# Kernel tuning notes

Hardware: AMD Instinct MI355X
Metric: run time of the kernel (lower is better)

Reference implementation:

```python
import math
import jax, jax.numpy as jnp
import numpy as np

HIDDEN = 768
N_HEADS = 12
HEAD_DIM = HIDDEN // N_HEADS


def _alibi_slopes(num_heads: int) -> np.ndarray:
    def pow2_slopes(n):
        start = 2.0 ** (-2.0 ** (-(math.log2(n) - 3)))
        return start ** np.arange(1, n + 1, dtype=np.float32)
    if math.log2(num_heads).is_integer():
        return pow2_slopes(num_heads).astype(np.float32)
    closest = 2 ** math.floor(math.log2(num_heads))
    base = pow2_slopes(closest)
    extra = pow2_slopes(2 * closest)[0::2][: num_heads - closest]
    return np.concatenate([base, extra], axis=0).astype(np.float32)

ALIBI_SLOPES = jnp.asarray(_alibi_slopes(N_HEADS))


def setup_inputs() -> dict:
    key = jax.random.key(0)
    ks = jax.random.split(key, 7)
    B, S = 4, 2048
    scale = 1.0 / math.sqrt(HIDDEN)
    inp = {
        "hidden_states": jax.random.normal(ks[0], (B, S, HIDDEN), dtype=jnp.float32),
        "Wq": jax.random.normal(ks[1], (HIDDEN, HIDDEN), dtype=jnp.float32) * scale,
        "bq": jnp.zeros((HIDDEN,), dtype=jnp.float32),
        "Wk": jax.random.normal(ks[2], (HIDDEN, HIDDEN), dtype=jnp.float32) * scale,
        "bk": jnp.zeros((HIDDEN,), dtype=jnp.float32),
        "Wv": jax.random.normal(ks[3], (HIDDEN, HIDDEN), dtype=jnp.float32) * scale,
        "bv": jnp.zeros((HIDDEN,), dtype=jnp.float32),
        "attention_mask": jnp.ones((B, S), dtype=jnp.int32),
    }
    return inp


def reference(hidden_states, Wq, bq, Wk, bk, Wv, bv, attention_mask):
    B, S, _ = hidden_states.shape
    H, D = N_HEADS, HEAD_DIM
    scaling = D ** (-0.5)

    # nn.Linear: x @ W.T + b, then split heads -> [B, S, H, D]
    q = (hidden_states @ Wq.T + bq).reshape(B, S, H, D)
    k = (hidden_states @ Wk.T + bk).reshape(B, S, H, D)
    v = (hidden_states @ Vv_fix(Wv, bv, hidden_states)) if False else (hidden_states @ Wv.T + bv).reshape(B, S, H, D)

    # scaled scores [B, H, Sq, Sk]
    scores = jnp.einsum("bqhd,bkhd->bhqk", q, k) * scaling

    # ALiBi bias: -slope[h] * |kv_idx - q_idx|
    pos = jnp.arange(S)
    dist = jnp.abs(pos[None, :] - pos[:, None]).astype(scores.dtype)  # [Sq, Sk]
    alibi = -ALIBI_SLOPES.astype(scores.dtype)[:, None, None] * dist  # [H, Sq, Sk]

    # padding mask over kv positions (additive min like score_mod)
    mask_penalty = jnp.finfo(scores.dtype).min
    mask_bias = jnp.where(attention_mask.astype(bool), 0.0, mask_penalty)  # [B, Sk]

    scores = scores + alibi[None] + mask_bias[:, None, None, :]
    probs = jax.nn.softmax(scores, axis=-1)

    out = jnp.einsum("bhqk,bkhd->bqhd", probs, v)  # [B, Sq, H, D]
    return out.reshape(B, S, H * D)  # dropout is no-op in eval


def Vv_fix(*a):  # unused helper kept trivially (never called)
    raise NotImplementedError
```

## Files before the change

kernel.cpp:

```cpp
#include <hip/hip_runtime.h>
#include <hip/hip_bf16.h>

#define HIDDEN 768
#define NH 12
#define HD 64
#define BB 4
#define SS 2048
#define M_TOT (BB * SS)
#define NQKV (3 * HIDDEN)
#define LOG2E 1.44269504f

typedef __attribute__((ext_vector_type(8))) short bf16x8;
typedef __attribute__((ext_vector_type(4))) float f32x4;
typedef __attribute__((ext_vector_type(4))) unsigned int u32x4;

__device__ inline unsigned short f2bf(float x) {
    __hip_bfloat16 h = __float2bfloat16(x);
    return *reinterpret_cast<unsigned short*>(&h);
}

__device__ inline void gl_lds16(const unsigned short* g, unsigned short* s) {
    __builtin_amdgcn_global_load_lds(
        (const __attribute__((address_space(1))) unsigned int*)g,
        (__attribute__((address_space(3))) unsigned int*)s, 16, 0, 0);
}

__device__ inline void bar_vm4() {
    __builtin_amdgcn_sched_barrier(0);
    asm volatile("s_waitcnt vmcnt(4)" ::: "memory");
    __builtin_amdgcn_s_barrier();
    __builtin_amdgcn_sched_barrier(0);
}
__device__ inline void bar_vm0() {
    __builtin_amdgcn_sched_barrier(0);
    asm volatile("s_waitcnt vmcnt(0)" ::: "memory");
    __builtin_amdgcn_s_barrier();
    __builtin_amdgcn_sched_barrier(0);
}

__global__ __launch_bounds__(256) void cast_kernel(
    const float* __restrict__ hs, const float* __restrict__ wq,
    const float* __restrict__ wk, const float* __restrict__ wv,
    const int* __restrict__ mask, unsigned short* __restrict__ a_bf,
    unsigned short* __restrict__ w_bf, float* __restrict__ mb,
    int* __restrict__ anym) {
    const int HS_N = M_TOT * HIDDEN / 4;
    const int W_N = HIDDEN * HIDDEN / 4;
    int idx = blockIdx.x * blockDim.x + threadIdx.x;
    if (idx < BB * SS) mb[idx] = mask[idx] ? 0.f : -1e30f;
    if (idx < BB * 32) {
        int b = idx >> 5, t = idx & 31;
        const int* mp = mask + b * SS + t * 64;
        int any = 0;
#pragma unroll 8
        for (int j = 0; j < 64; j++) any |= (mp[j] == 0);
        anym[idx] = any;
    }
    if (idx >= HS_N + 3 * W_N) return;
    if (idx < HS_N) {
        float4 v = ((const float4*)hs)[idx];
        ushort4 o;
        o.x = f2bf(v.x); o.y = f2bf(v.y); o.z = f2bf(v.z); o.w = f2bf(v.w);
        ((ushort4*)a_bf)[idx] = o;
    } else {
        int widx = idx - HS_N;
        const float* src;
        int off;
        if (widx < W_N)        { src = wq; off = widx; }
        else if (widx < 2*W_N) { src = wk; off = widx - W_N; }
        else                   { src = wv; off = widx - 2 * W_N; }
        float4 v = ((const float4*)src)[off];
        ushort4 o;
        o.x = f2bf(v.x); o.y = f2bf(v.y); o.z = f2bf(v.z); o.w = f2bf(v.w);
        ((ushort4*)w_bf)[widx] = o;
    }
}

__global__ __launch_bounds__(256, 3) void qkv_gemm(
    const unsigned short* __restrict__ A, const unsigned short* __restrict__ W,
    const float* __restrict__ bq, const float* __restrict__ bk,
    const float* __restrict__ bv, unsigned short* __restrict__ qbuf,
    unsigned short* __restrict__ kf, unsigned short* __restrict__ vf) {
    __shared__ unsigned short As[3][128][32];
    __shared__ unsigned short Bs[3][128][32];
    const int tid = threadIdx.x;
    const int flat = blockIdx.y * gridDim.x + blockIdx.x;
    const int xcd = flat & 7;
    const int qq = flat >> 3;
    const int mgrp = qq / 18;
    const int nidx = qq % 18;
    const int m0 = (mgrp * 8 + xcd) * 128;
    const int n0 = nidx * 128;
    const int w = tid >> 6, l = tid & 63;
    const int wm = w >> 1, wn = w & 1;
    const int lrow = l & 15;
    const int g4 = l >> 4;
    const int fcol = (g4 ^ (lrow >> 2)) * 8;

    const int srow = l >> 2;
    const int sslot = (l & 3) ^ ((l >> 4) & 3);
    const unsigned short* pA =
        A + (size_t)(m0 + w * 32 + srow) * HIDDEN + sslot * 8;
    const unsigned short* pB =
        W + (size_t)(n0 + w * 32 + srow) * HIDDEN + sslot * 8;

    f32x4 acc[4][4] = {};

#define STAGE(bb)                                          \
    do {                                                   \
        gl_lds16(pA,               &As[bb][w * 32][0]);    \
        gl_lds16(pA + 16 * HIDDEN, &As[bb][w * 32 + 16][0]); \
        gl_lds16(pB,               &Bs[bb][w * 32][0]);    \
        gl_lds16(pB + 16 * HIDDEN, &Bs[bb][w * 32 + 16][0]); \
        pA += 32; pB += 32;                                \
    } while (0)

    STAGE(0);
    STAGE(1);
    bar_vm4();
    int cur = 0;
    const int NKT = HIDDEN / 32;

    for (int kt = 0; kt < NKT; kt++) {
        if (kt + 2 < NKT) {
            int db = (cur >= 1) ? cur - 1 : 2;
            STAGE(db);
        }
        bf16x8 af[4], bfr[4];
#pragma unroll
        for (int mi = 0; mi < 4; mi++)
            af[mi] = *(const bf16x8*)&As[cur][wm * 64 + mi * 16 + lrow][fcol];
#pragma unroll
        for (int ni = 0; ni < 4; ni++)
            bfr[ni] = *(const bf16x8*)&Bs[cur][wn * 64 + ni * 16 + lrow][fcol];
        __builtin_amdgcn_s_setprio(1);
#pragma unroll
        for (int mi = 0; mi < 4; mi++)
#pragma unroll
            for (int ni = 0; ni < 4; ni++)
                acc[mi][ni] = __builtin_amdgcn_mfma_f32_16x16x32_bf16(
                    af[mi], bfr[ni], acc[mi][ni], 0, 0, 0);
        __builtin_amdgcn_s_setprio(0);
        if (kt < NKT - 1) {
            if (kt < NKT - 2) bar_vm4();
            else bar_vm0();
        }
        cur = (cur == 2) ? 0 : cur + 1;
    }
#undef STAGE

    if (n0 < 768) {
#pragma unroll
        for (int mi = 0; mi < 4; mi++) {
            const size_t rbase =
                (size_t)(m0 + wm * 64 + mi * 16 + g4 * 4) * 768;
#pragma unroll
            for (int ni = 0; ni < 4; ni++) {
                int col = n0 + wn * 64 + ni * 16 + lrow;
                float bias = bq[col];
#pragma unroll
                for (int i = 0; i < 4; i++)
                    qbuf[rbase + (size_t)i * 768 + col] =
                        f2bf((acc[mi][ni][i] + bias) * 0.125f);
            }
        }
    } else if (n0 < 1536) {
        const int bb2 = m0 >> 11;
        const int sbase = (m0 & 2047) + wm * 64 + g4 * 4;
        const int lsb = g4 * 4;
#pragma unroll
        for (int mi = 0; mi < 4; mi++) {
            const int kv16 = (sbase + mi * 16) >> 4;
#pragma unroll
            for (int ni = 0; ni < 4; ni++) {
                int dd = n0 - 768 + wn * 64 + ni * 16 + lrow;
                float bias = bk[dd];
                int hh = dd >> 6, d = dd & 63;
                int gk2 = d >> 3, d8 = d & 7;
                size_t base = ((size_t)(bb2 * NH + hh) * 128 + kv16) * 1024 +
                              (gk2 * 16 + lsb) * 8 + d8;
#pragma unroll
                for (int i = 0; i < 4; i++)
                    kf[base + i * 8] = f2bf(acc[mi][ni][i] + bias);
            }
        }
    } else {
        const int bb2 = m0 >> 11;
#pragma unroll
        for (int mi = 0; mi < 4; mi++) {
            const int s0r = (m0 & 2047) + wm * 64 + mi * 16 + g4 * 4;
            const int kv32 = s0r >> 5, gv = (s0r >> 3) & 3, s8 = s0r & 7;
#pragma unroll
            for (int ni = 0; ni < 4; ni++) {
                int dd = n0 - 1536 + wn * 64 + ni * 16 + lrow;
                float bias = bv[dd];
                int hh = dd >> 6, d = dd & 63;
                int dm = d >> 4, lr = d & 15;
                ushort4 o;
                o.x = f2bf(acc[mi][ni][0] + bias);
                o.y = f2bf(acc[mi][ni][1] + bias);
                o.z = f2bf(acc[mi][ni][2] + bias);
                o.w = f2bf(acc[mi][ni][3] + bias);
                *(ushort4*)(vf + (((size_t)(bb2 * NH + hh) * 4 + dm) * 64 + kv32) * 512 +
                            (gv * 16 + lr) * 8 + s8) = o;
            }
        }
    }
}

__global__ __launch_bounds__(256) void attn_kernel(
    const unsigned short* __restrict__ Qb, const unsigned short* __restrict__ KF,
    const unsigned short* __restrict__ VF, const float* __restrict__ MB,
    const int* __restrict__ ANYM, float* __restrict__ out) {
    __shared__ unsigned short Kl[2][4096];
    __shared__ unsigned short Vl[2][4096];

    const int head_order[12] = {7, 6, 5, 4, 3, 11, 2, 10, 1, 9, 0, 8};
    const int Rtab[12]       = {31, 17, 9, 5, 3, 2, 2, 1, 1, 1, 1, 1};

    const int tid = threadIdx.x;
    const int w = tid >> 6, l = tid & 63;
    const int flat = blockIdx.y * gridDim.x + blockIdx.x;
    const int xcd = flat & 7;
    const int rem = flat >> 3;
    const int slot = rem >> 5;
    const int qt = rem & 31;
    const int byy = slot * 8 + xcd;
    const int hidx = byy >> 2;
    const int b = byy & 3;
    const int h = head_order[hidx];
    const int R = Rtab[hidx];
    const int bh = b * NH + h;
    const int lrow = l & 15;
    const int g = l >> 4;
    const int q = qt * 64 + w * 16 + lrow;
    const int l8 = l * 8;

    const float slope = (h < 8) ? exp2f(-(float)(h + 1))
                                : exp2f(-((float)(h - 8) + 0.5f));
    const float nslope2 = -slope * LOG2E;
    const float stp = 64.f * nslope2;

    const unsigned short* qp = Qb + (size_t)(b * SS + q) * 768 + h * HD + g * 8;
    const bf16x8 qf0 = *(const bf16x8*)(qp);
    const bf16x8 qf1 = *(const bf16x8*)(qp + 32);

    const unsigned short* kfb = KF + (size_t)bh * 128 * 1024;
    const unsigned short* vfb = VF + (size_t)bh * 4 * 64 * 512;
    const float* mbp = MB + b * SS + g * 4;
    const int* anyp = ANYM + b * 32;

    bf16x8 ones;
#pragma unroll
    for (int j = 0; j < 8; j++) ones[j] = (short)0x3F80;

    f32x4 accT[4] = {};
    f32x4 lacc = {};
    float m_run = 14.0f;
    float ta[16];
    bool need_full = true;

    const int kt_lo = max(0, qt - R);
    const int kt_hi = min(31, qt + R);

    {
        const unsigned short* gk0 = kfb + ((size_t)kt_lo * 4 + w) * 1024 + l8;
        const unsigned short* gv0 = vfb + ((size_t)w * 64 + kt_lo * 2) * 512 + l8;
        gl_lds16(gk0,       &Kl[0][w * 1024]);
        gl_lds16(gk0 + 512, &Kl[0][w * 1024 + 512]);
        gl_lds16(gv0,       &Vl[0][w * 1024]);
        gl_lds16(gv0 + 512, &Vl[0][w * 1024 + 512]);
    }
    __syncthreads();

    const unsigned short* gk = kfb + ((size_t)(kt_lo + 1) * 4 + w) * 1024 + l8;
    const unsigned short* gv = vfb + ((size_t)w * 64 + (size_t)(kt_lo + 1) * 2) * 512 + l8;
    int cur = 0;

    for (int kt = kt_lo; kt <= kt_hi; kt++) {
        if (kt < kt_hi) {
            gl_lds16(gk,       &Kl[cur ^ 1][w * 1024]);
            gl_lds16(gk + 512, &Kl[cur ^ 1][w * 1024 + 512]);
            gl_lds16(gv,       &Vl[cur ^ 1][w * 1024]);
            gl_lds16(gv + 512, &Vl[cur ^ 1][w * 1024 + 512]);
            gk += 4096;
            gv += 1024;
        }

        f32x4 s4[4];
        __builtin_amdgcn_s_setprio(1);
#pragma unroll
        for (int nf = 0; nf < 4; nf++) {
            bf16x8 k0 = *(const bf16x8*)&Kl[cur][nf * 1024 + l8];
            bf16x8 k1 = *(const bf16x8*)&Kl[cur][nf * 1024 + 512 + l8];
            f32x4 z = {};
            z = __builtin_amdgcn_mfma_f32_16x16x32_bf16(k0, qf0, z, 0, 0, 0);
            z = __builtin_amdgcn_mfma_f32_16x16x32_bf16(k1, qf1, z, 0, 0, 0);
            s4[nf] = z;
        }
        __builtin_amdgcn_s_setprio(0);

        if (need_full || kt == qt || kt == qt + 1) {
            const float fdf = (float)(kt * 64 + g * 4 - q);
#pragma unroll
            for (int nf = 0; nf < 4; nf++)
#pragma unroll
                for (int i = 0; i < 4; i++)
                    ta[nf * 4 + i] = fabsf(fdf + (float)(nf * 16 + i)) * nslope2;
        } else {
            const float d = (kt > qt) ? stp : -stp;
#pragma unroll
            for (int e = 0; e < 16; e++) ta[e] += d;
        }
        need_full = false;

        float sv[16];
#pragma unroll
        for (int nf = 0; nf < 4; nf++)
#pragma unroll
            for (int i = 0; i < 4; i++)
                sv[nf * 4 + i] = fmaf(s4[nf][i], LOG2E, ta[nf * 4 + i]);
        if (anyp[kt]) {
#pragma unroll
            for (int nf = 0; nf < 4; nf++) {
                float4 mbv = *(const float4*)(mbp + kt * 64 + nf * 16);
                sv[nf * 4 + 0] += mbv.x;
                sv[nf * 4 + 1] += mbv.y;
                sv[nf * 4 + 2] += mbv.z;
                sv[nf * 4 + 3] += mbv.w;
            }
        }

        float t0 = fmaxf(fmaxf(sv[0], sv[1]), sv[2]);
        float t1 = fmaxf(fmaxf(sv[3], sv[4]), sv[5]);
        float t2 = fmaxf(fmaxf(sv[6], sv[7]), sv[8]);
        float t3 = fmaxf(fmaxf(sv[9], sv[10]), sv[11]);
        float t4 = fmaxf(fmaxf(sv[12], sv[13]), sv[14]);
        float mt = fmaxf(fmaxf(fmaxf(t0, t1), fmaxf(t2, t3)), fmaxf(t4, sv[15]));

        if (!__all(mt <= m_run + 8.0f)) {
            mt = fmaxf(mt, __shfl_xor(mt, 16));
            mt = fmaxf(mt, __shfl_xor(mt, 32));
            mt = fmaxf(mt, __shfl_xor(mt, 1));
            mt = fmaxf(mt, __shfl_xor(mt, 2));
            mt = fmaxf(mt, __shfl_xor(mt, 4));
            mt = fmaxf(mt, __shfl_xor(mt, 8));
            float mnew = fmaxf(m_run, mt);
            float corr = __builtin_amdgcn_exp2f(m_run - mnew);
            m_run = mnew;
#pragma unroll
            for (int i = 0; i < 4; i++) lacc[i] *= corr;
#pragma unroll
            for (int m = 0; m < 4; m++)
#pragma unroll
                for (int i = 0; i < 4; i++) accT[m][i] *= corr;
        }

        float p[16];
#pragma unroll
        for (int e = 0; e < 16; e++)
            p[e] = __builtin_amdgcn_exp2f(sv[e] - m_run);

        unsigned pk[4][2];
#pragma unroll
        for (int nf = 0; nf < 4; nf++) {
            asm("v_cvt_pk_bf16_f32 %0, %1, %2"
                : "=v"(pk[nf][0]) : "v"(p[nf * 4 + 0]), "v"(p[nf * 4 + 1]));
            asm("v_cvt_pk_bf16_f32 %0, %1, %2"
                : "=v"(pk[nf][1]) : "v"(p[nf * 4 + 2]), "v"(p[nf * 4 + 3]));
        }

        const int dstA = ((((g & 1) << 1) | (g >> 1)) << 4) | lrow;
        const int idxA = dstA << 2;
        const int idxB = idxA ^ 128;
        const bool odd = (g & 1);
        unsigned rA0 = __builtin_amdgcn_ds_permute(idxA, (int)(odd ? pk[1][0] : pk[0][0]));
        unsigned rA1 = __builtin_amdgcn_ds_permute(idxA, (int)(odd ? pk[1][1] : pk[0][1]));
        unsigned rB0 = __builtin_amdgcn_ds_permute(idxB, (int)(odd ? pk[0][0] : pk[1][0]));
        unsigned rB1 = __builtin_amdgcn_ds_permute(idxB, (int)(odd ? pk[0][1] : pk[1][1]));
        unsigned rA2 = __builtin_amdgcn_ds_permute(idxA, (int)(odd ? pk[3][0] : pk[2][0]));
        unsigned rA3 = __builtin_amdgcn_ds_permute(idxA, (int)(odd ? pk[3][1] : pk[2][1]));
        unsigned rB2 = __builtin_amdgcn_ds_permute(idxB, (int)(odd ? pk[2][0] : pk[3][0]));
        unsigned rB3 = __builtin_amdgcn_ds_permute(idxB, (int)(odd ? pk[2][1] : pk[3][1]));
        const bool hi = (g >> 1);
        u32x4 uf0, uf1;
        uf0.x = hi ? rB0 : rA0; uf0.y = hi ? rB1 : rA1;
        uf0.z = hi ? rA0 : rB0; uf0.w = hi ? rA1 : rB1;
        uf1.x = hi ? rB2 : rA2; uf1.y = hi ? rB3 : rA3;
        uf1.z = hi ? rA2 : rB2; uf1.w = hi ? rA3 : rB3;
        bf16x8 pf0 = __builtin_bit_cast(bf16x8, uf0);
        bf16x8 pf1 = __builtin_bit_cast(bf16x8, uf1);

        __builtin_amdgcn_s_setprio(1);
#pragma unroll
        for (int m = 0; m < 4; m++) {
            bf16x8 v0 = *(const bf16x8*)&Vl[cur][m * 1024 + l8];
            bf16x8 v1 = *(const bf16x8*)&Vl[cur][m * 1024 + 512 + l8];
            accT[m] = __builtin_amdgcn_mfma_f32_16x16x32_bf16(v0, pf0, accT[m], 0, 0, 0);
            accT[m] = __builtin_amdgcn_mfma_f32_16x16x32_bf16(v1, pf1, accT[m], 0, 0, 0);
        }
        lacc = __builtin_amdgcn_mfma_f32_16x16x32_bf16(ones, pf0, lacc, 0, 0, 0);
        lacc = __builtin_amdgcn_mfma_f32_16x16x32_bf16(ones, pf1, lacc, 0, 0, 0);
        __builtin_amdgcn_s_setprio(0);

        __syncthreads();
        cur ^= 1;
    }

    const float inv = 1.0f / lacc[0];
    float* op = out + (size_t)(b * SS + q) * HIDDEN + h * HD + g * 4;
#pragma unroll
    for (int m = 0; m < 4; m++) {
        float4 o;
        o.x = accT[m][0] * inv; o.y = accT[m][1] * inv;
        o.z = accT[m][2] * inv; o.w = accT[m][3] * inv;
        *(float4*)(op + m * 16) = o;
    }
}

extern "C" void kernel_launch(void* const* d_in, const int* in_sizes, int n_in,
                              void* d_out, int out_size, void* d_ws,
                              size_t ws_size, hipStream_t stream) {
    const float* hs = (const float*)d_in[0];
    const float* wq = (const float*)d_in[1];
    const float* bq = (const float*)d_in[2];
    const float* wk = (const float*)d_in[3];
    const float* bk = (const float*)d_in[4];
    const float* wv = (const float*)d_in[5];
    const float* bv = (const float*)d_in[6];
    const int* mask = (const int*)d_in[7];
    float* out = (float*)d_out;

    unsigned short* a_bf = (unsigned short*)d_ws;
    unsigned short* w_bf = a_bf + (size_t)M_TOT * HIDDEN;
    unsigned short* qbuf = w_bf + (size_t)NQKV * HIDDEN;
    unsigned short* kf = qbuf + (size_t)M_TOT * 768;
    unsigned short* vf = kf + (size_t)BB * NH * 128 * 1024;
    float* mb = (float*)(vf + (size_t)BB * NH * 4 * 64 * 512);
    int* anym = (int*)(mb + BB * SS);

    int castN = (M_TOT * HIDDEN + 3 * HIDDEN * HIDDEN) / 4;
    cast_kernel<<<(castN + 255) / 256, 256, 0, stream>>>(
        hs, wq, wk, wv, mask, a_bf, w_bf, mb, anym);

    dim3 ggrid(NQKV / 128, M_TOT / 128);
    qkv_gemm<<<ggrid, 256, 0, stream>>>(a_bf, w_bf, bq, bk, bv, qbuf, kf, vf);

    dim3 agrid(SS / 64, NH * BB);
    attn_kernel<<<agrid, 256, 0, stream>>>(qbuf, kf, vf, mb, anym, out);
}
```

Measured before the change: 102.1 us.

## Enlarge QKV GEMM tile to 256x128 with 512 threads and double buffering

Each QKV projection GEMM block now covers 256 rows of the activation matrix instead of 128, using 8 waves, so every staged weight tile is reused by twice as many rows. The three-stage LDS ring with explicit vmcnt waits is replaced by a two-buffer scheme synchronised with __syncthreads. This cuts redundant weight loads and halves the block count. The trade-off is shallower prefetch: each iteration now waits for all outstanding loads, which can expose global-memory latency. Larger blocks may also lower occupancy.

```diff
diff --git a/kernel.cpp b/kernel.cpp
--- a/kernel.cpp
+++ b/kernel.cpp
@@ -23,19 +23,6 @@
     __builtin_amdgcn_global_load_lds(
         (const __attribute__((address_space(1))) unsigned int*)g,
         (__attribute__((address_space(3))) unsigned int*)s, 16, 0, 0);
-}
-
-__device__ inline void bar_vm4() {
-    __builtin_amdgcn_sched_barrier(0);
-    asm volatile("s_waitcnt vmcnt(4)" ::: "memory");
-    __builtin_amdgcn_s_barrier();
-    __builtin_amdgcn_sched_barrier(0);
-}
-__device__ inline void bar_vm0() {
-    __builtin_amdgcn_sched_barrier(0);
-    asm volatile("s_waitcnt vmcnt(0)" ::: "memory");
-    __builtin_amdgcn_s_barrier();
-    __builtin_amdgcn_sched_barrier(0);
 }
 
 __global__ __launch_bounds__(256) void cast_kernel(
@@ -76,20 +63,20 @@
     }
 }
 
-__global__ __launch_bounds__(256, 3) void qkv_gemm(
+__global__ __launch_bounds__(512, 6) void qkv_gemm(
     const unsigned short* __restrict__ A, const unsigned short* __restrict__ W,
     const float* __restrict__ bq, const float* __restrict__ bk,
     const float* __restrict__ bv, unsigned short* __restrict__ qbuf,
     unsigned short* __restrict__ kf, unsigned short* __restrict__ vf) {
-    __shared__ unsigned short As[3][128][32];
-    __shared__ unsigned short Bs[3][128][32];
+    __shared__ unsigned short As[2][256][32];
+    __shared__ unsigned short Bs[2][128][32];
     const int tid = threadIdx.x;
     const int flat = blockIdx.y * gridDim.x + blockIdx.x;
     const int xcd = flat & 7;
     const int qq = flat >> 3;
     const int mgrp = qq / 18;
     const int nidx = qq % 18;
-    const int m0 = (mgrp * 8 + xcd) * 128;
+    const int m0 = (mgrp * 8 + xcd) * 256;
     const int n0 = nidx * 128;
     const int w = tid >> 6, l = tid & 63;
     const int wm = w >> 1, wn = w & 1;
@@ -102,30 +89,25 @@
     const unsigned short* pA =
         A + (size_t)(m0 + w * 32 + srow) * HIDDEN + sslot * 8;
     const unsigned short* pB =
-        W + (size_t)(n0 + w * 32 + srow) * HIDDEN + sslot * 8;
+        W + (size_t)(n0 + w * 16 + srow) * HIDDEN + sslot * 8;
 
     f32x4 acc[4][4] = {};
 
-#define STAGE(bb)                                          \
-    do {                                                   \
-        gl_lds16(pA,               &As[bb][w * 32][0]);    \
+#define STAGE(bb)                                            \
+    do {                                                     \
+        gl_lds16(pA,               &As[bb][w * 32][0]);      \
         gl_lds16(pA + 16 * HIDDEN, &As[bb][w * 32 + 16][0]); \
-        gl_lds16(pB,               &Bs[bb][w * 32][0]);    \
-        gl_lds16(pB + 16 * HIDDEN, &Bs[bb][w * 32 + 16][0]); \
-        pA += 32; pB += 32;                                \
+        gl_lds16(pB,               &Bs[bb][w * 16][0]);      \
+        pA += 32; pB += 32;                                  \
     } while (0)
 
     STAGE(0);
-    STAGE(1);
-    bar_vm4();
+    __syncthreads();
     int cur = 0;
     const int NKT = HIDDEN / 32;
 
     for (int kt = 0; kt < NKT; kt++) {
-        if (kt + 2 < NKT) {
-            int db = (cur >= 1) ? cur - 1 : 2;
-            STAGE(db);
-        }
+        if (kt < NKT - 1) STAGE(cur ^ 1);
         bf16x8 af[4], bfr[4];
 #pragma unroll
         for (int mi = 0; mi < 4; mi++)
@@ -141,11 +123,8 @@
                 acc[mi][ni] = __builtin_amdgcn_mfma_f32_16x16x32_bf16(
                     af[mi], bfr[ni], acc[mi][ni], 0, 0, 0);
         __builtin_amdgcn_s_setprio(0);
-        if (kt < NKT - 1) {
-            if (kt < NKT - 2) bar_vm4();
-            else bar_vm0();
-        }
-        cur = (cur == 2) ? 0 : cur + 1;
+        __syncthreads();
+        cur ^= 1;
     }
 #undef STAGE
 
@@ -443,8 +422,8 @@
     cast_kernel<<<(castN + 255) / 256, 256, 0, stream>>>(
         hs, wq, wk, wv, mask, a_bf, w_bf, mb, anym);
 
-    dim3 ggrid(NQKV / 128, M_TOT / 128);
-    qkv_gemm<<<ggrid, 256, 0, stream>>>(a_bf, w_bf, bq, bk, bv, qbuf, kf, vf);
+    dim3 ggrid(18, 32);
+    qkv_gemm<<<ggrid, 512, 0, stream>>>(a_bf, w_bf, bq, bk, bv, qbuf, kf, vf);
 
     dim3 agrid(SS / 64, NH * BB);
     attn_kernel<<<agrid, 256, 0, stream>>>(qbuf, kf, vf, mb, anym, out);
```

New measurement: 386.2 us. 3.78x slower.
